# Kernel tuning notes

Measured on AMD Instinct MI355X. Metric: run time of the kernel, lower is better.

Reference implementation:

```python
import jax, jax.numpy as jnp
import numpy as np

N_NODES = 200_000
N_BONDS = 200_000
N_EDGES = 2 * N_BONDS
D_V, D_E, D_H, DEPTH = 133, 14, 200, 3


def setup_inputs() -> dict:
    key = jax.random.key(0)
    ks = jax.random.split(key, 10)
    V = jax.random.normal(ks[0], (N_NODES, D_V), dtype=jnp.float32)
    E_feat = jax.random.normal(ks[1], (N_EDGES, D_E), dtype=jnp.float32)
    # paired directed edges: edge 2b = (u,v), edge 2b+1 = (v,u)
    u = jax.random.randint(ks[2], (N_BONDS,), 0, N_NODES)
    v = jax.random.randint(ks[3], (N_BONDS,), 0, N_NODES)
    src = jnp.stack([u, v], axis=1).reshape(-1)
    dst = jnp.stack([v, u], axis=1).reshape(-1)
    edge_index = jnp.stack([src, dst], axis=0).astype(jnp.int64)
    rev_edge_index = (jnp.arange(N_EDGES) ^ 1).astype(jnp.int64)
    s = 0.05
    W_i = jax.random.normal(ks[4], (D_V + D_E, D_H), dtype=jnp.float32) * s
    b_i = jax.random.normal(ks[5], (D_H,), dtype=jnp.float32) * s
    W_h = jax.random.normal(ks[6], (D_H, D_H), dtype=jnp.float32) * s
    b_h = jax.random.normal(ks[7], (D_H,), dtype=jnp.float32) * s
    W_o = jax.random.normal(ks[8], (D_V + D_H, D_H), dtype=jnp.float32) * s
    b_o = jax.random.normal(ks[9], (D_H,), dtype=jnp.float32) * s
    return {"V": V, "E_feat": E_feat, "edge_index": edge_index,
            "rev_edge_index": rev_edge_index, "W_i": W_i, "b_i": b_i,
            "W_h": W_h, "b_h": b_h, "W_o": W_o, "b_o": b_o}


def reference(V, E_feat, edge_index, rev_edge_index, W_i, b_i, W_h, b_h, W_o, b_o):
    src = edge_index[0]
    dst = edge_index[1]
    n_edges = E_feat.shape[0]
    # h^(0) = relu(W_i([x_v || e_vw]))
    H0 = jax.nn.relu(jnp.concatenate([V[src], E_feat], axis=1) @ W_i + b_i)
    H = H0
    not_self_rev = (rev_edge_index != jnp.arange(n_edges))[:, None]  # [E,1]
    for _ in range(1, DEPTH):
        node_messages = jax.ops.segment_sum(H, dst, num_segments=N_NODES)  # [N,d_h]
        M = node_messages[src] - jnp.where(not_self_rev, H[rev_edge_index], 0.0)
        H = jax.nn.relu(H0 + M @ W_h + b_h)
    M_v = jax.ops.segment_sum(H, src, num_segments=N_NODES)  # [N,d_h]
    H_v = jax.nn.relu(jnp.concatenate([V, M_v], axis=1) @ W_o + b_o)
    return H_v
```

## Files before the change

### kernel.cpp

```cpp
#include <hip/hip_runtime.h>
#include <hip/hip_bf16.h>
#include <stdint.h>

typedef __hip_bfloat16 bf16;
typedef __attribute__((ext_vector_type(8))) short short8;
typedef __attribute__((ext_vector_type(4))) float f32x4;

#define NN 200000
#define NNPAD 200064
#define NE 400000
#define DV 133
#define DE 14
#define DH 200
#define MT 128
#define NT 13
#define LDA 40
#define NCH 782

#define KI 160
#define KH 224
#define KO 352
#define LDV 160

#define MFMA(a, b, c) __builtin_amdgcn_mfma_f32_16x16x32_bf16((a), (b), (c), 0, 0, 0)

__device__ __forceinline__ float us2f(unsigned short u) {
  return __uint_as_float(((unsigned)u) << 16);
}
__device__ __forceinline__ unsigned short f2us(float f) {
  bf16 h = __float2bfloat16(f);
  return *reinterpret_cast<unsigned short*>(&h);
}

__global__ __launch_bounds__(256) void prepw_kernel(
    const float* __restrict__ W, int K, int ldk, bf16* __restrict__ out)
{
  int idx = blockIdx.x * 256 + threadIdx.x;
  int rowv = ldk >> 3;
  int total = 208 * rowv;
  if (idx >= total) return;
  int c = idx / rowv, r = idx - c * rowv;
  int k0 = r * 8;
  short8 w;
#pragma unroll
  for (int j = 0; j < 8; ++j) {
    int k = k0 + j;
    float v = (k < K && c < DH) ? W[(size_t)k * DH + c] : 0.f;
    w[j] = (short)f2us(v);
  }
  *(short8*)&((unsigned short*)out)[(size_t)c * ldk + k0] = w;
}

__global__ __launch_bounds__(256) void prepwo_kernel(
    const float* __restrict__ Wo, bf16* __restrict__ out)
{
  int idx = blockIdx.x * 256 + threadIdx.x;
  int total = 208 * (KO >> 3);
  if (idx >= total) return;
  int c = idx / (KO >> 3), r = idx - c * (KO >> 3);
  int k0 = r * 8;
  short8 w;
#pragma unroll
  for (int j = 0; j < 8; ++j) {
    int k = k0 + j;
    int sr = (k < 200) ? (133 + k) : (k - 200);
    float v = (k < 333 && c < DH) ? Wo[(size_t)sr * DH + c] : 0.f;
    w[j] = (short)f2us(v);
  }
  *(short8*)&((unsigned short*)out)[(size_t)c * KO + k0] = w;
}

__global__ __launch_bounds__(256) void packv_kernel(
    const float* __restrict__ V, unsigned short* __restrict__ Vb)
{
  int idx = blockIdx.x * 256 + threadIdx.x;
  if (idx >= NN * (LDV / 8)) return;
  int n = idx / (LDV / 8), g = idx - n * (LDV / 8);
  int k0 = g * 8;
  short8 w;
#pragma unroll
  for (int j = 0; j < 8; ++j) {
    int k = k0 + j;
    float v = (k < DV) ? V[(size_t)n * DV + k] : 0.f;
    w[j] = (short)f2us(v);
  }
  *(short8*)&Vb[(size_t)n * LDV + k0] = w;
}

__global__ __launch_bounds__(256) void packav_kernel(
    const float* __restrict__ V, unsigned short* __restrict__ Abuf)
{
  int idx = blockIdx.x * 256 + threadIdx.x;
  if (idx >= NNPAD * (KO / 8)) return;
  int n = idx / (KO / 8), g = idx - n * (KO / 8);
  int k0 = g * 8;
  if (n < NN && k0 < 200) return;
  short8 w;
#pragma unroll
  for (int j = 0; j < 8; ++j) {
    int k = k0 + j;
    float v = (n < NN && k >= 200 && k < 333) ? V[(size_t)n * DV + (k - 200)] : 0.f;
    w[j] = (short)f2us(v);
  }
  *(short8*)&Abuf[(size_t)n * KO + k0] = w;
}

__global__ __launch_bounds__(256) void hist_kernel(
    const int* __restrict__ dst, int* __restrict__ counts)
{
  int e = blockIdx.x * 256 + threadIdx.x;
  if (e < NE) atomicAdd(&counts[dst[e]], 1);
}

__global__ __launch_bounds__(256) void chunksum_kernel(
    const int* __restrict__ counts, int* __restrict__ chunkSum)
{
  int b = blockIdx.x, tid = threadIdx.x;
  int i = b * 256 + tid;
  int v = (i < NN) ? counts[i] : 0;
#pragma unroll
  for (int d = 32; d; d >>= 1) v += __shfl_down(v, d, 64);
  __shared__ int ws[4];
  if ((tid & 63) == 0) ws[tid >> 6] = v;
  __syncthreads();
  if (tid == 0) chunkSum[b] = ws[0] + ws[1] + ws[2] + ws[3];
}

__global__ __launch_bounds__(1024) void scanchunks_kernel(
    const int* __restrict__ chunkSum, int* __restrict__ chunkOff)
{
  __shared__ int s[1024];
  int tid = threadIdx.x;
  int v = (tid < NCH) ? chunkSum[tid] : 0;
  s[tid] = v;
  __syncthreads();
  for (int d = 1; d < 1024; d <<= 1) {
    int t = (tid >= d) ? s[tid - d] : 0;
    __syncthreads();
    s[tid] += t;
    __syncthreads();
  }
  if (tid < NCH) chunkOff[tid] = s[tid] - v;
}

__global__ __launch_bounds__(256) void scanlocal_kernel(
    const int* __restrict__ counts, const int* __restrict__ chunkOff,
    int* __restrict__ offsets, int* __restrict__ cursor)
{
  __shared__ int s[256];
  int b = blockIdx.x, tid = threadIdx.x;
  int i = b * 256 + tid;
  int v = (i < NN) ? counts[i] : 0;
  s[tid] = v;
  __syncthreads();
  for (int d = 1; d < 256; d <<= 1) {
    int t = (tid >= d) ? s[tid - d] : 0;
    __syncthreads();
    s[tid] += t;
    __syncthreads();
  }
  if (i < NN) {
    int off = chunkOff[b] + s[tid] - v;
    offsets[i] = off;
    cursor[i] = off;
  }
  if (i == 0) offsets[NN] = NE;
}

__global__ __launch_bounds__(256) void scatter_kernel(
    const int* __restrict__ dst, int* __restrict__ cursor, int* __restrict__ perm)
{
  int e = blockIdx.x * 256 + threadIdx.x;
  if (e < NE) {
    int p = atomicAdd(&cursor[dst[e]], 1);
    perm[p] = e;
  }
}

__global__ __launch_bounds__(256) void h0_kernel(
    const unsigned short* __restrict__ Vb,
    const float* __restrict__ Ef,
    const int* __restrict__ src,
    const bf16* __restrict__ WiT,
    const float* __restrict__ bi,
    bf16* __restrict__ H0)
{
  __shared__ __align__(16) unsigned short AsS[MT * LDA];
  __shared__ __align__(16) unsigned short WtS[208 * LDA];
  __shared__ int Ssrc[MT];
  __shared__ float Sb[DH];
  const int tid = threadIdx.x;
  const int e0 = blockIdx.x * MT;
  if (tid < MT) Ssrc[tid] = src[e0 + tid];
  if (tid < DH) Sb[tid] = bi[tid];
  const int wv = tid >> 6, ln = tid & 15, q = (tid & 63) >> 4;
  f32x4 acc[NT][2];
#pragma unroll
  for (int t = 0; t < NT; ++t)
#pragma unroll
    for (int m = 0; m < 2; ++m) acc[t][m] = (f32x4){0.f, 0.f, 0.f, 0.f};
  const unsigned short* Wp = (const unsigned short*)WiT;
  __syncthreads();
  for (int k0 = 0; k0 < 128; k0 += 32) {
    for (int idx = tid; idx < 832; idx += 256) {
      int c = idx >> 2, kg = idx & 3;
      *(short8*)&WtS[c * LDA + kg * 8] =
          *(const short8*)&Wp[(size_t)c * KI + k0 + kg * 8];
    }
    for (int idx = tid; idx < 512; idx += 256) {
      int rr = idx >> 2, kg = idx & 3;
      int s = Ssrc[rr];
      *(short8*)&AsS[rr * LDA + kg * 8] =
          *(const short8*)&Vb[(size_t)s * LDV + k0 + kg * 8];
    }
    __syncthreads();
    {
      short8 a0 = *(const short8*)&AsS[(wv * 32 + ln) * LDA + q * 8];
      short8 a1 = *(const short8*)&AsS[(wv * 32 + 16 + ln) * LDA + q * 8];
#pragma unroll
      for (int t = 0; t < NT; ++t) {
        short8 b = *(const short8*)&WtS[(t * 16 + ln) * LDA + q * 8];
        acc[t][0] = MFMA(a0, b, acc[t][0]);
        acc[t][1] = MFMA(a1, b, acc[t][1]);
      }
    }
    __syncthreads();
  }
  {
    const int k0 = 128;
    for (int idx = tid; idx < 832; idx += 256) {
      int c = idx >> 2, kg = idx & 3;
      *(short8*)&WtS[c * LDA + kg * 8] =
          *(const short8*)&Wp[(size_t)c * KI + k0 + kg * 8];
    }
    {
      int rr = tid >> 1, half = tid & 1;
      int e = e0 + rr, s = Ssrc[rr];
      int kb = k0 + half * 16;
      unsigned short av[16];
#pragma unroll
      for (int j = 0; j < 16; ++j) {
        int k = kb + j;
        unsigned short x = 0;
        if (k < DV) x = Vb[(size_t)s * LDV + k];
        else if (k < DV + DE) x = f2us(Ef[(size_t)e * DE + (k - DV)]);
        av[j] = x;
      }
      short8 w0, w1;
#pragma unroll
      for (int j = 0; j < 8; ++j) { w0[j] = (short)av[j]; w1[j] = (short)av[8 + j]; }
      *(short8*)&AsS[rr * LDA + half * 16] = w0;
      *(short8*)&AsS[rr * LDA + half * 16 + 8] = w1;
    }
    __syncthreads();
    {
      short8 a0 = *(const short8*)&AsS[(wv * 32 + ln) * LDA + q * 8];
      short8 a1 = *(const short8*)&AsS[(wv * 32 + 16 + ln) * LDA + q * 8];
#pragma unroll
      for (int t = 0; t < NT; ++t) {
        short8 b = *(const short8*)&WtS[(t * 16 + ln) * LDA + q * 8];
        acc[t][0] = MFMA(a0, b, acc[t][0]);
        acc[t][1] = MFMA(a1, b, acc[t][1]);
      }
    }
    __syncthreads();
  }
#pragma unroll
  for (int t = 0; t < NT; ++t) {
    int c = t * 16 + ln;
    if (c < DH) {
#pragma unroll
      for (int m = 0; m < 2; ++m)
#pragma unroll
        for (int i = 0; i < 4; ++i) {
          int e = e0 + wv * 32 + m * 16 + q * 4 + i;
          float h = acc[t][m][i] + Sb[c];
          H0[(size_t)e * DH + c] = __float2bfloat16(h > 0.f ? h : 0.f);
        }
    }
  }
}

__global__ __launch_bounds__(256) void gemmq_kernel(
    const bf16* __restrict__ H,
    const bf16* __restrict__ WhT,
    bf16* __restrict__ Q)
{
  __shared__ __align__(16) unsigned short AsS[MT * LDA];
  __shared__ __align__(16) unsigned short WtS[208 * LDA];
  const int tid = threadIdx.x;
  const int e0 = blockIdx.x * MT;
  const int wv = tid >> 6, ln = tid & 15, q = (tid & 63) >> 4;
  f32x4 acc[NT][2];
#pragma unroll
  for (int t = 0; t < NT; ++t)
#pragma unroll
    for (int m = 0; m < 2; ++m) acc[t][m] = (f32x4){0.f, 0.f, 0.f, 0.f};
  const unsigned short* Hs = (const unsigned short*)H;
  const unsigned short* Wp = (const unsigned short*)WhT;
  for (int k0 = 0; k0 < KH; k0 += 32) {
    for (int idx = tid; idx < 832; idx += 256) {
      int c = idx >> 2, kg = idx & 3;
      *(short8*)&WtS[c * LDA + kg * 8] =
          *(const short8*)&Wp[(size_t)c * KH + k0 + kg * 8];
    }
    for (int idx = tid; idx < 512; idx += 256) {
      int rr = idx >> 2, kg = idx & 3;
      *(short8*)&AsS[rr * LDA + kg * 8] =
          *(const short8*)&Hs[(size_t)(e0 + rr) * DH + k0 + kg * 8];
    }
    __syncthreads();
    {
      short8 a0 = *(const short8*)&AsS[(wv * 32 + ln) * LDA + q * 8];
      short8 a1 = *(const short8*)&AsS[(wv * 32 + 16 + ln) * LDA + q * 8];
#pragma unroll
      for (int t = 0; t < NT; ++t) {
        short8 b = *(const short8*)&WtS[(t * 16 + ln) * LDA + q * 8];
        acc[t][0] = MFMA(a0, b, acc[t][0]);
        acc[t][1] = MFMA(a1, b, acc[t][1]);
      }
    }
    __syncthreads();
  }
#pragma unroll
  for (int t = 0; t < NT; ++t) {
    int c = t * 16 + ln;
    if (c < DH) {
#pragma unroll
      for (int m = 0; m < 2; ++m)
#pragma unroll
        for (int i = 0; i < 4; ++i) {
          int e = e0 + wv * 32 + m * 16 + q * 4 + i;
          Q[(size_t)e * DH + c] = __float2bfloat16(acc[t][m][i]);
        }
    }
  }
}

__global__ __launch_bounds__(256) void fusedmp_kernel(
    const bf16* __restrict__ Q, const bf16* H0,
    const int* __restrict__ offsets, const int* __restrict__ perm,
    const float* __restrict__ bh, bf16* Hout)
{
  int t = blockIdx.x * 256 + threadIdx.x;
  if (t >= NN * 25) return;
  int n = t / 25, g = t - n * 25;
  int st = offsets[n], en = offsets[n + 1];
  if (st == en) return;
  const unsigned short* Qs = (const unsigned short*)Q;
  const unsigned short* H0s = (const unsigned short*)H0;
  unsigned short* Os = (unsigned short*)Hout;
  float a[8];
  const float4* bp = (const float4*)(bh + g * 8);
  float4 b0 = bp[0], b1 = bp[1];
  a[0] = b0.x; a[1] = b0.y; a[2] = b0.z; a[3] = b0.w;
  a[4] = b1.x; a[5] = b1.y; a[6] = b1.z; a[7] = b1.w;
  for (int j = st; j < en; ++j) {
    int e = perm[j];
    short8 u = *(const short8*)(Qs + (size_t)e * DH + g * 8);
#pragma unroll
    for (int k = 0; k < 8; ++k) a[k] += us2f((unsigned short)u[k]);
  }
  for (int j = st; j < en; ++j) {
    int e = perm[j];
    int eo = e ^ 1;
    short8 uq = *(const short8*)(Qs + (size_t)e * DH + g * 8);
    short8 uh = *(const short8*)(H0s + (size_t)eo * DH + g * 8);
    short8 w;
#pragma unroll
    for (int k = 0; k < 8; ++k) {
      float h = a[k] - us2f((unsigned short)uq[k]) + us2f((unsigned short)uh[k]);
      w[k] = (short)f2us(h > 0.f ? h : 0.f);
    }
    *(short8*)(Os + (size_t)eo * DH + g * 8) = w;
  }
}

__global__ __launch_bounds__(256) void gather_kernel(
    const bf16* __restrict__ H, const int* __restrict__ offsets,
    const int* __restrict__ perm, int xm, unsigned short* __restrict__ Abuf)
{
  int t = blockIdx.x * 256 + threadIdx.x;
  if (t >= NN * 25) return;
  int n = t / 25, g = t - n * 25;
  int st = offsets[n], en = offsets[n + 1];
  float a[8];
#pragma unroll
  for (int k = 0; k < 8; ++k) a[k] = 0.f;
  const unsigned short* Hs = (const unsigned short*)H;
  for (int j = st; j < en; ++j) {
    int e = perm[j] ^ xm;
    short8 u = *(const short8*)(Hs + (size_t)e * DH + g * 8);
#pragma unroll
    for (int k = 0; k < 8; ++k) a[k] += us2f((unsigned short)u[k]);
  }
  short8 w;
#pragma unroll
  for (int k = 0; k < 8; ++k) w[k] = (short)f2us(a[k]);
  *(short8*)&Abuf[(size_t)n * KO + g * 8] = w;
}

__global__ __launch_bounds__(256) void out_kernel(
    const unsigned short* __restrict__ Abuf,
    const bf16* __restrict__ WoT,
    const float* __restrict__ bo,
    float* __restrict__ out)
{
  __shared__ __align__(16) unsigned short AsS[MT * LDA];
  __shared__ __align__(16) unsigned short WtS[208 * LDA];
  __shared__ float Sb[DH];
  const int tid = threadIdx.x;
  const int n0 = blockIdx.x * MT;
  if (tid < DH) Sb[tid] = bo[tid];
  const int wv = tid >> 6, ln = tid & 15, q = (tid & 63) >> 4;
  f32x4 acc[NT][2];
#pragma unroll
  for (int t = 0; t < NT; ++t)
#pragma unroll
    for (int m = 0; m < 2; ++m) acc[t][m] = (f32x4){0.f, 0.f, 0.f, 0.f};
  const unsigned short* Wp = (const unsigned short*)WoT;
  __syncthreads();
  for (int k0 = 0; k0 < KO; k0 += 32) {
    for (int idx = tid; idx < 832; idx += 256) {
      int c = idx >> 2, kg = idx & 3;
      *(short8*)&WtS[c * LDA + kg * 8] =
          *(const short8*)&Wp[(size_t)c * KO + k0 + kg * 8];
    }
    for (int idx = tid; idx < 512; idx += 256) {
      int rr = idx >> 2, kg = idx & 3;
      *(short8*)&AsS[rr * LDA + kg * 8] =
          *(const short8*)&Abuf[(size_t)(n0 + rr) * KO + k0 + kg * 8];
    }
    __syncthreads();
    {
      short8 a0 = *(const short8*)&AsS[(wv * 32 + ln) * LDA + q * 8];
      short8 a1 = *(const short8*)&AsS[(wv * 32 + 16 + ln) * LDA + q * 8];
#pragma unroll
      for (int t = 0; t < NT; ++t) {
        short8 b = *(const short8*)&WtS[(t * 16 + ln) * LDA + q * 8];
        acc[t][0] = MFMA(a0, b, acc[t][0]);
        acc[t][1] = MFMA(a1, b, acc[t][1]);
      }
    }
    __syncthreads();
  }
#pragma unroll
  for (int t = 0; t < NT; ++t) {
    int c = t * 16 + ln;
    if (c < DH) {
#pragma unroll
      for (int m = 0; m < 2; ++m)
#pragma unroll
        for (int i = 0; i < 4; ++i) {
          int n = n0 + wv * 32 + m * 16 + q * 4 + i;
          if (n < NN) {
            float h = acc[t][m][i] + Sb[c];
            out[(size_t)n * DH + c] = h > 0.f ? h : 0.f;
          }
        }
    }
  }
}

extern "C" void kernel_launch(void* const* d_in, const int* in_sizes, int n_in,
                              void* d_out, int out_size, void* d_ws, size_t ws_size,
                              hipStream_t stream)
{
  const float* V  = (const float*)d_in[0];
  const float* Ef = (const float*)d_in[1];
  const int* eidx = (const int*)d_in[2];
  const int* rev  = (const int*)d_in[3];   (void)rev;
  const float* Wi = (const float*)d_in[4];
  const float* bi = (const float*)d_in[5];
  const float* Wh = (const float*)d_in[6];
  const float* bh = (const float*)d_in[7];
  const float* Wo = (const float*)d_in[8];
  const float* bo = (const float*)d_in[9];
  const int* src = eidx;
  const int* dst = eidx + NE;

  bf16* H0 = (bf16*)d_ws;
  bf16* Hb = H0 + (size_t)NE * DH;
  bf16* Q  = Hb + (size_t)NE * DH;
  unsigned short* Vb16 = (unsigned short*)Hb;
  unsigned short* Abuf = (unsigned short*)Q;
  int* counts   = (int*)(Q + (size_t)NE * DH);
  int* chunkSum = counts + NN;
  int* chunkOff = chunkSum + 1024;
  int* offsets  = chunkOff + 1024;
  int* cursor   = offsets + NN + 1;
  int* perm     = cursor + NN;
  bf16* WiT = (bf16*)(((uintptr_t)(perm + NE) + 15) & ~(uintptr_t)15);
  bf16* WhT = WiT + 208 * KI;
  bf16* WoT = WhT + 208 * KH;

  const int gGE = NE / MT;
  const int gON = (NN + MT - 1) / MT;
  const int gE  = (NE + 255) / 256;
  const int gN  = (NN + 255) / 256;
  const int gG  = (NN * 25 + 255) / 256;

  hipMemsetAsync(counts, 0, (size_t)NN * sizeof(int), stream);
  hist_kernel<<<gE, 256, 0, stream>>>(dst, counts);
  chunksum_kernel<<<NCH, 256, 0, stream>>>(counts, chunkSum);
  scanchunks_kernel<<<1, 1024, 0, stream>>>(chunkSum, chunkOff);
  scanlocal_kernel<<<gN, 256, 0, stream>>>(counts, chunkOff, offsets, cursor);
  scatter_kernel<<<gE, 256, 0, stream>>>(dst, cursor, perm);

  prepw_kernel<<<(208 * KI / 8 + 255) / 256, 256, 0, stream>>>(Wi, DV + DE, KI, WiT);
  prepw_kernel<<<(208 * KH / 8 + 255) / 256, 256, 0, stream>>>(Wh, DH, KH, WhT);
  prepwo_kernel<<<(208 * KO / 8 + 255) / 256, 256, 0, stream>>>(Wo, WoT);

  packv_kernel<<<(NN * (LDV / 8) + 255) / 256, 256, 0, stream>>>(V, Vb16);

  h0_kernel<<<gGE, 256, 0, stream>>>(Vb16, Ef, src, WiT, bi, H0);

  gemmq_kernel<<<gGE, 256, 0, stream>>>(H0, WhT, Q);
  fusedmp_kernel<<<gG, 256, 0, stream>>>(Q, H0, offsets, perm, bh, Hb);

  gemmq_kernel<<<gGE, 256, 0, stream>>>(Hb, WhT, Q);
  fusedmp_kernel<<<gG, 256, 0, stream>>>(Q, H0, offsets, perm, bh, H0);

  packav_kernel<<<(NNPAD * (KO / 8) + 255) / 256, 256, 0, stream>>>(V, Abuf);

  gather_kernel<<<gG, 256, 0, stream>>>(H0, offsets, perm, 1, Abuf);
  out_kernel<<<gON, 256, 0, stream>>>(Abuf, WoT, bo, (float*)d_out);
}
```

Before: 1.370 ms.

## Prepack weights into MFMA fragment order and load operands directly from global

Weights are repacked into per-lane MFMA B-fragment order so each wave loads B operands directly from global/L2 instead of staging through shared memory. A operands are also read directly from global rows, removing LDS tiles and the per-chunk barriers in the h0, gemmq and out GEMMs. A new packing kernel precomputes the tail chunk of the h0 input (last V columns plus edge features) in bf16. The cost is redundant B loads across waves that depend on cache hits, plus an extra pass over edges.

After: 1.283 ms. 6.3% less time.

```diff
diff --git a/kernel.cpp b/kernel.cpp
--- a/kernel.cpp
+++ b/kernel.cpp
@@ -14,11 +14,11 @@
 #define DH 200
 #define MT 128
 #define NT 13
-#define LDA 40
 #define NCH 782
 
-#define KI 160
-#define KH 224
+#define CI 5
+#define CH 7
+#define CO 11
 #define KO 352
 #define LDV 160
 
@@ -32,42 +32,35 @@
   return *reinterpret_cast<unsigned short*>(&h);
 }
 
-__global__ __launch_bounds__(256) void prepw_kernel(
-    const float* __restrict__ W, int K, int ldk, bf16* __restrict__ out)
-{
-  int idx = blockIdx.x * 256 + threadIdx.x;
-  int rowv = ldk >> 3;
-  int total = 208 * rowv;
-  if (idx >= total) return;
-  int c = idx / rowv, r = idx - c * rowv;
-  int k0 = r * 8;
+__global__ __launch_bounds__(256) void prepwpack_kernel(
+    const float* __restrict__ W, int Ksrc, int nchunks, int mode,
+    unsigned short* __restrict__ out)
+{
+  int f = blockIdx.x * 256 + threadIdx.x;
+  int total = nchunks * 13 * 64;
+  if (f >= total) return;
+  int c = f / 832, rem = f - c * 832;
+  int t = rem >> 6, l = rem & 63;
+  int q = l >> 4, ln = l & 15;
+  int col = t * 16 + ln;
   short8 w;
 #pragma unroll
   for (int j = 0; j < 8; ++j) {
-    int k = k0 + j;
-    float v = (k < K && c < DH) ? W[(size_t)k * DH + c] : 0.f;
+    int k = c * 32 + q * 8 + j;
+    float v = 0.f;
+    if (col < DH) {
+      if (mode == 0) {
+        if (k < Ksrc) v = W[(size_t)k * DH + col];
+      } else {
+        if (k < 333) {
+          int sr = (k < 200) ? (133 + k) : (k - 200);
+          v = W[(size_t)sr * DH + col];
+        }
+      }
+    }
     w[j] = (short)f2us(v);
   }
-  *(short8*)&((unsigned short*)out)[(size_t)c * ldk + k0] = w;
-}
-
-__global__ __launch_bounds__(256) void prepwo_kernel(
-    const float* __restrict__ Wo, bf16* __restrict__ out)
-{
-  int idx = blockIdx.x * 256 + threadIdx.x;
-  int total = 208 * (KO >> 3);
-  if (idx >= total) return;
-  int c = idx / (KO >> 3), r = idx - c * (KO >> 3);
-  int k0 = r * 8;
-  short8 w;
-#pragma unroll
-  for (int j = 0; j < 8; ++j) {
-    int k = k0 + j;
-    int sr = (k < 200) ? (133 + k) : (k - 200);
-    float v = (k < 333 && c < DH) ? Wo[(size_t)sr * DH + c] : 0.f;
-    w[j] = (short)f2us(v);
-  }
-  *(short8*)&((unsigned short*)out)[(size_t)c * KO + k0] = w;
+  *(short8*)&out[(size_t)f * 8] = w;
 }
 
 __global__ __launch_bounds__(256) void packv_kernel(
@@ -85,6 +78,32 @@
     w[j] = (short)f2us(v);
   }
   *(short8*)&Vb[(size_t)n * LDV + k0] = w;
+}
+
+__global__ __launch_bounds__(256) void packet_kernel(
+    const float* __restrict__ V, const float* __restrict__ Ef,
+    const int* __restrict__ src, unsigned short* __restrict__ Et)
+{
+  int idx = blockIdx.x * 256 + threadIdx.x;
+  if (idx >= NE * 4) return;
+  int e = idx >> 2, part = idx & 3;
+  short8 w;
+#pragma unroll
+  for (int j = 0; j < 8; ++j) w[j] = 0;
+  if (part == 0) {
+    int s = src[e];
+#pragma unroll
+    for (int j = 0; j < 5; ++j) w[j] = (short)f2us(V[(size_t)s * DV + 128 + j]);
+#pragma unroll
+    for (int j = 5; j < 8; ++j) w[j] = (short)f2us(Ef[(size_t)e * DE + (j - 5)]);
+  } else if (part == 1) {
+#pragma unroll
+    for (int j = 0; j < 8; ++j) w[j] = (short)f2us(Ef[(size_t)e * DE + 3 + j]);
+  } else if (part == 2) {
+#pragma unroll
+    for (int j = 0; j < 3; ++j) w[j] = (short)f2us(Ef[(size_t)e * DE + 11 + j]);
+  }
+  *(short8*)&Et[(size_t)e * 32 + part * 8] = w;
 }
 
 __global__ __launch_bounds__(256) void packav_kernel(
@@ -179,91 +198,54 @@
 
 __global__ __launch_bounds__(256) void h0_kernel(
     const unsigned short* __restrict__ Vb,
-    const float* __restrict__ Ef,
+    const unsigned short* __restrict__ Et,
     const int* __restrict__ src,
-    const bf16* __restrict__ WiT,
+    const unsigned short* __restrict__ Bp,
     const float* __restrict__ bi,
     bf16* __restrict__ H0)
 {
-  __shared__ __align__(16) unsigned short AsS[MT * LDA];
-  __shared__ __align__(16) unsigned short WtS[208 * LDA];
-  __shared__ int Ssrc[MT];
   __shared__ float Sb[DH];
   const int tid = threadIdx.x;
   const int e0 = blockIdx.x * MT;
-  if (tid < MT) Ssrc[tid] = src[e0 + tid];
   if (tid < DH) Sb[tid] = bi[tid];
   const int wv = tid >> 6, ln = tid & 15, q = (tid & 63) >> 4;
+  const int lane = tid & 63;
+  __syncthreads();
   f32x4 acc[NT][2];
 #pragma unroll
   for (int t = 0; t < NT; ++t)
 #pragma unroll
     for (int m = 0; m < 2; ++m) acc[t][m] = (f32x4){0.f, 0.f, 0.f, 0.f};
-  const unsigned short* Wp = (const unsigned short*)WiT;
-  __syncthreads();
-  for (int k0 = 0; k0 < 128; k0 += 32) {
-    for (int idx = tid; idx < 832; idx += 256) {
-      int c = idx >> 2, kg = idx & 3;
-      *(short8*)&WtS[c * LDA + kg * 8] =
-          *(const short8*)&Wp[(size_t)c * KI + k0 + kg * 8];
-    }
-    for (int idx = tid; idx < 512; idx += 256) {
-      int rr = idx >> 2, kg = idx & 3;
-      int s = Ssrc[rr];
-      *(short8*)&AsS[rr * LDA + kg * 8] =
-          *(const short8*)&Vb[(size_t)s * LDV + k0 + kg * 8];
-    }
-    __syncthreads();
-    {
-      short8 a0 = *(const short8*)&AsS[(wv * 32 + ln) * LDA + q * 8];
-      short8 a1 = *(const short8*)&AsS[(wv * 32 + 16 + ln) * LDA + q * 8];
-#pragma unroll
-      for (int t = 0; t < NT; ++t) {
-        short8 b = *(const short8*)&WtS[(t * 16 + ln) * LDA + q * 8];
-        acc[t][0] = MFMA(a0, b, acc[t][0]);
-        acc[t][1] = MFMA(a1, b, acc[t][1]);
-      }
-    }
-    __syncthreads();
+  const int r0 = wv * 32 + ln;
+  const int s0 = src[e0 + r0], s1 = src[e0 + r0 + 16];
+  const unsigned short* v0p = Vb + (size_t)s0 * LDV;
+  const unsigned short* v1p = Vb + (size_t)s1 * LDV;
+  const unsigned short* bp = Bp + (size_t)lane * 8;
+  short8 bfr[NT];
+#pragma unroll
+  for (int c = 0; c < 4; ++c) {
+    short8 a0 = *(const short8*)(v0p + c * 32 + q * 8);
+    short8 a1 = *(const short8*)(v1p + c * 32 + q * 8);
+#pragma unroll
+    for (int t = 0; t < NT; ++t)
+      bfr[t] = *(const short8*)(bp + (size_t)(c * NT + t) * 512);
+#pragma unroll
+    for (int t = 0; t < NT; ++t) {
+      acc[t][0] = MFMA(a0, bfr[t], acc[t][0]);
+      acc[t][1] = MFMA(a1, bfr[t], acc[t][1]);
+    }
   }
   {
-    const int k0 = 128;
-    for (int idx = tid; idx < 832; idx += 256) {
-      int c = idx >> 2, kg = idx & 3;
-      *(short8*)&WtS[c * LDA + kg * 8] =
-          *(const short8*)&Wp[(size_t)c * KI + k0 + kg * 8];
-    }
-    {
-      int rr = tid >> 1, half = tid & 1;
-      int e = e0 + rr, s = Ssrc[rr];
-      int kb = k0 + half * 16;
-      unsigned short av[16];
-#pragma unroll
-      for (int j = 0; j < 16; ++j) {
-        int k = kb + j;
-        unsigned short x = 0;
-        if (k < DV) x = Vb[(size_t)s * LDV + k];
-        else if (k < DV + DE) x = f2us(Ef[(size_t)e * DE + (k - DV)]);
-        av[j] = x;
-      }
-      short8 w0, w1;
-#pragma unroll
-      for (int j = 0; j < 8; ++j) { w0[j] = (short)av[j]; w1[j] = (short)av[8 + j]; }
-      *(short8*)&AsS[rr * LDA + half * 16] = w0;
-      *(short8*)&AsS[rr * LDA + half * 16 + 8] = w1;
-    }
-    __syncthreads();
-    {
-      short8 a0 = *(const short8*)&AsS[(wv * 32 + ln) * LDA + q * 8];
-      short8 a1 = *(const short8*)&AsS[(wv * 32 + 16 + ln) * LDA + q * 8];
-#pragma unroll
-      for (int t = 0; t < NT; ++t) {
-        short8 b = *(const short8*)&WtS[(t * 16 + ln) * LDA + q * 8];
-        acc[t][0] = MFMA(a0, b, acc[t][0]);
-        acc[t][1] = MFMA(a1, b, acc[t][1]);
-      }
-    }
-    __syncthreads();
+    short8 a0 = *(const short8*)(Et + (size_t)(e0 + r0) * 32 + q * 8);
+    short8 a1 = *(const short8*)(Et + (size_t)(e0 + r0 + 16) * 32 + q * 8);
+#pragma unroll
+    for (int t = 0; t < NT; ++t)
+      bfr[t] = *(const short8*)(bp + (size_t)(4 * NT + t) * 512);
+#pragma unroll
+    for (int t = 0; t < NT; ++t) {
+      acc[t][0] = MFMA(a0, bfr[t], acc[t][0]);
+      acc[t][1] = MFMA(a1, bfr[t], acc[t][1]);
+    }
   }
 #pragma unroll
   for (int t = 0; t < NT; ++t) {
@@ -283,44 +265,35 @@
 
 __global__ __launch_bounds__(256) void gemmq_kernel(
     const bf16* __restrict__ H,
-    const bf16* __restrict__ WhT,
+    const unsigned short* __restrict__ Bp,
     bf16* __restrict__ Q)
 {
-  __shared__ __align__(16) unsigned short AsS[MT * LDA];
-  __shared__ __align__(16) unsigned short WtS[208 * LDA];
   const int tid = threadIdx.x;
   const int e0 = blockIdx.x * MT;
   const int wv = tid >> 6, ln = tid & 15, q = (tid & 63) >> 4;
+  const int lane = tid & 63;
   f32x4 acc[NT][2];
 #pragma unroll
   for (int t = 0; t < NT; ++t)
 #pragma unroll
     for (int m = 0; m < 2; ++m) acc[t][m] = (f32x4){0.f, 0.f, 0.f, 0.f};
   const unsigned short* Hs = (const unsigned short*)H;
-  const unsigned short* Wp = (const unsigned short*)WhT;
-  for (int k0 = 0; k0 < KH; k0 += 32) {
-    for (int idx = tid; idx < 832; idx += 256) {
-      int c = idx >> 2, kg = idx & 3;
-      *(short8*)&WtS[c * LDA + kg * 8] =
-          *(const short8*)&Wp[(size_t)c * KH + k0 + kg * 8];
-    }
-    for (int idx = tid; idx < 512; idx += 256) {
-      int rr = idx >> 2, kg = idx & 3;
-      *(short8*)&AsS[rr * LDA + kg * 8] =
-          *(const short8*)&Hs[(size_t)(e0 + rr) * DH + k0 + kg * 8];
-    }
-    __syncthreads();
-    {
-      short8 a0 = *(const short8*)&AsS[(wv * 32 + ln) * LDA + q * 8];
-      short8 a1 = *(const short8*)&AsS[(wv * 32 + 16 + ln) * LDA + q * 8];
-#pragma unroll
-      for (int t = 0; t < NT; ++t) {
-        short8 b = *(const short8*)&WtS[(t * 16 + ln) * LDA + q * 8];
-        acc[t][0] = MFMA(a0, b, acc[t][0]);
-        acc[t][1] = MFMA(a1, b, acc[t][1]);
-      }
-    }
-    __syncthreads();
+  const unsigned short* a0p = Hs + (size_t)(e0 + wv * 32 + ln) * DH;
+  const unsigned short* a1p = a0p + (size_t)16 * DH;
+  const unsigned short* bp = Bp + (size_t)lane * 8;
+  short8 bfr[NT];
+#pragma unroll
+  for (int c = 0; c < CH; ++c) {
+    short8 a0 = *(const short8*)(a0p + c * 32 + q * 8);
+    short8 a1 = *(const short8*)(a1p + c * 32 + q * 8);
+#pragma unroll
+    for (int t = 0; t < NT; ++t)
+      bfr[t] = *(const short8*)(bp + (size_t)(c * NT + t) * 512);
+#pragma unroll
+    for (int t = 0; t < NT; ++t) {
+      acc[t][0] = MFMA(a0, bfr[t], acc[t][0]);
+      acc[t][1] = MFMA(a1, bfr[t], acc[t][1]);
+    }
   }
 #pragma unroll
   for (int t = 0; t < NT; ++t) {
@@ -402,47 +375,38 @@
 
 __global__ __launch_bounds__(256) void out_kernel(
     const unsigned short* __restrict__ Abuf,
-    const bf16* __restrict__ WoT,
+    const unsigned short* __restrict__ Bp,
     const float* __restrict__ bo,
     float* __restrict__ out)
 {
-  __shared__ __align__(16) unsigned short AsS[MT * LDA];
-  __shared__ __align__(16) unsigned short WtS[208 * LDA];
   __shared__ float Sb[DH];
   const int tid = threadIdx.x;
   const int n0 = blockIdx.x * MT;
   if (tid < DH) Sb[tid] = bo[tid];
   const int wv = tid >> 6, ln = tid & 15, q = (tid & 63) >> 4;
+  const int lane = tid & 63;
+  __syncthreads();
   f32x4 acc[NT][2];
 #pragma unroll
   for (int t = 0; t < NT; ++t)
 #pragma unroll
     for (int m = 0; m < 2; ++m) acc[t][m] = (f32x4){0.f, 0.f, 0.f, 0.f};
-  const unsigned short* Wp = (const unsigned short*)WoT;
-  __syncthreads();
-  for (int k0 = 0; k0 < KO; k0 += 32) {
-    for (int idx = tid; idx < 832; idx += 256) {
-      int c = idx >> 2, kg = idx & 3;
-      *(short8*)&WtS[c * LDA + kg * 8] =
-          *(const short8*)&Wp[(size_t)c * KO + k0 + kg * 8];
-    }
-    for (int idx = tid; idx < 512; idx += 256) {
-      int rr = idx >> 2, kg = idx & 3;
-      *(short8*)&AsS[rr * LDA + kg * 8] =
-          *(const short8*)&Abuf[(size_t)(n0 + rr) * KO + k0 + kg * 8];
-    }
-    __syncthreads();
-    {
-      short8 a0 = *(const short8*)&AsS[(wv * 32 + ln) * LDA + q * 8];
-      short8 a1 = *(const short8*)&AsS[(wv * 32 + 16 + ln) * LDA + q * 8];
-#pragma unroll
-      for (int t = 0; t < NT; ++t) {
-        short8 b = *(const short8*)&WtS[(t * 16 + ln) * LDA + q * 8];
-        acc[t][0] = MFMA(a0, b, acc[t][0]);
-        acc[t][1] = MFMA(a1, b, acc[t][1]);
-      }
-    }
-    __syncthreads();
+  const unsigned short* a0p = Abuf + (size_t)(n0 + wv * 32 + ln) * KO;
+  const unsigned short* a1p = a0p + (size_t)16 * KO;
+  const unsigned short* bp = Bp + (size_t)lane * 8;
+  short8 bfr[NT];
+#pragma unroll
+  for (int c = 0; c < CO; ++c) {
+    short8 a0 = *(const short8*)(a0p + c * 32 + q * 8);
+    short8 a1 = *(const short8*)(a1p + c * 32 + q * 8);
+#pragma unroll
+    for (int t = 0; t < NT; ++t)
+      bfr[t] = *(const short8*)(bp + (size_t)(c * NT + t) * 512);
+#pragma unroll
+    for (int t = 0; t < NT; ++t) {
+      acc[t][0] = MFMA(a0, bfr[t], acc[t][0]);
+      acc[t][1] = MFMA(a1, bfr[t], acc[t][1]);
+    }
   }
 #pragma unroll
   for (int t = 0; t < NT; ++t) {
@@ -483,6 +447,7 @@
   bf16* Hb = H0 + (size_t)NE * DH;
   bf16* Q  = Hb + (size_t)NE * DH;
   unsigned short* Vb16 = (unsigned short*)Hb;
+  unsigned short* Et   = (unsigned short*)Q;
   unsigned short* Abuf = (unsigned short*)Q;
   int* counts   = (int*)(Q + (size_t)NE * DH);
   int* chunkSum = counts + NN;
@@ -490,9 +455,9 @@
   int* offsets  = chunkOff + 1024;
   int* cursor   = offsets + NN + 1;
   int* perm     = cursor + NN;
-  bf16* WiT = (bf16*)(((uintptr_t)(perm + NE) + 15) & ~(uintptr_t)15);
-  bf16* WhT = WiT + 208 * KI;
-  bf16* WoT = WhT + 208 * KH;
+  unsigned short* Bpi = (unsigned short*)(((uintptr_t)(perm + NE) + 15) & ~(uintptr_t)15);
+  unsigned short* Bph = Bpi + (size_t)CI * 832 * 8;
+  unsigned short* Bpo = Bph + (size_t)CH * 832 * 8;
 
   const int gGE = NE / MT;
   const int gON = (NN + MT - 1) / MT;
@@ -507,22 +472,23 @@
   scanlocal_kernel<<<gN, 256, 0, stream>>>(counts, chunkOff, offsets, cursor);
   scatter_kernel<<<gE, 256, 0, stream>>>(dst, cursor, perm);
 
-  prepw_kernel<<<(208 * KI / 8 + 255) / 256, 256, 0, stream>>>(Wi, DV + DE, KI, WiT);
-  prepw_kernel<<<(208 * KH / 8 + 255) / 256, 256, 0, stream>>>(Wh, DH, KH, WhT);
-  prepwo_kernel<<<(208 * KO / 8 + 255) / 256, 256, 0, stream>>>(Wo, WoT);
+  prepwpack_kernel<<<(CI * 832 + 255) / 256, 256, 0, stream>>>(Wi, DV + DE, CI, 0, Bpi);
+  prepwpack_kernel<<<(CH * 832 + 255) / 256, 256, 0, stream>>>(Wh, DH, CH, 0, Bph);
+  prepwpack_kernel<<<(CO * 832 + 255) / 256, 256, 0, stream>>>(Wo, 0, CO, 1, Bpo);
 
   packv_kernel<<<(NN * (LDV / 8) + 255) / 256, 256, 0, stream>>>(V, Vb16);
-
-  h0_kernel<<<gGE, 256, 0, stream>>>(Vb16, Ef, src, WiT, bi, H0);
-
-  gemmq_kernel<<<gGE, 256, 0, stream>>>(H0, WhT, Q);
+  packet_kernel<<<(NE * 4 + 255) / 256, 256, 0, stream>>>(V, Ef, src, Et);
+
+  h0_kernel<<<gGE, 256, 0, stream>>>(Vb16, Et, src, Bpi, bi, H0);
+
+  gemmq_kernel<<<gGE, 256, 0, stream>>>(H0, Bph, Q);
   fusedmp_kernel<<<gG, 256, 0, stream>>>(Q, H0, offsets, perm, bh, Hb);
 
-  gemmq_kernel<<<gGE, 256, 0, stream>>>(Hb, WhT, Q);
+  gemmq_kernel<<<gGE, 256, 0, stream>>>(Hb, Bph, Q);
   fusedmp_kernel<<<gG, 256, 0, stream>>>(Q, H0, offsets, perm, bh, H0);
 
   packav_kernel<<<(NNPAD * (KO / 8) + 255) / 256, 256, 0, stream>>>(V, Abuf);
 
   gather_kernel<<<gG, 256, 0, stream>>>(H0, offsets, perm, 1, Abuf);
-  out_kernel<<<gON, 256, 0, stream>>>(Abuf, WoT, bo, (float*)d_out);
-}
+  out_kernel<<<gON, 256, 0, stream>>>(Abuf, Bpo, bo, (float*)d_out);
+}
```
